# Optimization experiments

Hardware: AMD Instinct MI355X
Metric: run time of the kernel (lower is better)

Reference implementation:

```python
import jax, jax.numpy as jnp
import numpy as np

B, D, H, C, HALT_H, MAX_STEPS = 8192, 2048, 1024, 1000, 32, 10
EPS = 1e-08


def setup_inputs() -> dict:
    key = jax.random.key(0)
    ks = jax.random.split(key, 12)
    s = 0.02
    return {
        "x": jax.random.normal(ks[0], (B, D), jnp.float32),
        "enc_W": jax.random.normal(ks[1], (H, D), jnp.float32) * s,
        "enc_b": jnp.zeros((H,), jnp.float32),
        "ln_g": jnp.ones((H,), jnp.float32),
        "ln_b": jnp.zeros((H,), jnp.float32),
        "W_ih": jax.random.normal(ks[2], (3 * H, H), jnp.float32) * s,
        "W_hh": jax.random.normal(ks[3], (3 * H, H), jnp.float32) * s,
        "b_ih": jnp.zeros((3 * H,), jnp.float32),
        "b_hh": jnp.zeros((3 * H,), jnp.float32),
        "cls_W": jax.random.normal(ks[4], (C, H), jnp.float32) * s,
        "cls_b": jnp.zeros((C,), jnp.float32),
        "h1_W": jax.random.normal(ks[5], (HALT_H, H), jnp.float32) * s,
        "h1_b": jnp.zeros((HALT_H,), jnp.float32),
        "h2_W": jax.random.normal(ks[6], (1, HALT_H), jnp.float32) * s,
        "h2_b": jnp.zeros((1,), jnp.float32),
    }


def _forward(x, enc_W, enc_b, ln_g, ln_b, W_ih, W_hh, b_ih, b_hh,
             cls_W, cls_b, h1_W, h1_b, h2_W, h2_b):
    # encoder: Linear -> LayerNorm -> GELU (exact)
    z = x @ enc_W.T + enc_b
    mu = jnp.mean(z, axis=-1, keepdims=True)
    var = jnp.var(z, axis=-1, keepdims=True)
    z = (z - mu) * jax.lax.rsqrt(var + 1e-05) * ln_g + ln_b
    h0 = jax.nn.gelu(z, approximate=False)

    def step(h, _):
        gi = h @ W_ih.T + b_ih   # GRUCell with input = hidden
        gh = h @ W_hh.T + b_hh
        gi_r, gi_z, gi_n = jnp.split(gi, 3, axis=-1)
        gh_r, gh_z, gh_n = jnp.split(gh, 3, axis=-1)
        r = jax.nn.sigmoid(gi_r + gh_r)
        zt = jax.nn.sigmoid(gi_z + gh_z)
        n = jnp.tanh(gi_n + r * gh_n)
        h_new = (1.0 - zt) * n + zt * h
        logits = h_new @ cls_W.T + cls_b                         # [B, C]
        halt = jax.nn.sigmoid(
            jax.nn.relu(h_new @ h1_W.T + h1_b) @ h2_W.T + h2_b
        )[:, 0]                                                   # [B]
        return h_new, (logits, halt)

    _, (logits_steps, halt_steps) = jax.lax.scan(step, h0, None, length=MAX_STEPS)
    logits_stack = jnp.transpose(logits_steps, (1, 0, 2))  # [B, T, C]
    halts_stack = jnp.transpose(halt_steps, (1, 0))        # [B, T]

    log_not_halt = jnp.log(1.0 - halts_stack + EPS)
    cumsum_log = jnp.cumsum(log_not_halt, axis=1)
    cumsum_shifted = jnp.concatenate(
        [jnp.zeros((halts_stack.shape[0], 1), halts_stack.dtype), cumsum_log[:, :-1]], axis=1)
    halt_dist = halts_stack * jnp.exp(cumsum_shifted)
    remainder = 1.0 - jnp.sum(halt_dist, axis=1, keepdims=True)
    halt_dist = jnp.concatenate(
        [halt_dist[:, :-1], halt_dist[:, -1:] + jnp.maximum(remainder, 0.0)], axis=1)

    weighted_logits = jnp.sum(halt_dist[:, :, None] * logits_stack, axis=1)  # [B, C]
    step_indices = jnp.arange(1, MAX_STEPS + 1, dtype=weighted_logits.dtype)
    expected_steps = jnp.sum(halt_dist * step_indices, axis=1)
    probs = jax.nn.softmax(weighted_logits, axis=1)
    softmax_conf = jnp.max(probs, axis=1)
    comp_uncertainty = expected_steps / MAX_STEPS
    confidence = 0.7 * softmax_conf + 0.3 * (1.0 - comp_uncertainty)
    return (weighted_logits, probs, confidence, softmax_conf,
            expected_steps, halt_dist, comp_uncertainty)


def reference(x, enc_W, enc_b, ln_g, ln_b, W_ih, W_hh, b_ih, b_hh,
              cls_W, cls_b, h1_W, h1_b, h2_W, h2_b):
    return _forward(x, enc_W, enc_b, ln_g, ln_b, W_ih, W_hh, b_ih, b_hh,
                    cls_W, cls_b, h1_W, h1_b, h2_W, h2_b)
```

## Files before the change

### kernel.cpp

```cpp
#include <hip/hip_runtime.h>
#include <hip/hip_bf16.h>

#define B_ 8192
#define D_ 2048
#define H_ 1024
#define C_ 1000
#define NSTEP 10

typedef __attribute__((ext_vector_type(8))) short short8;
typedef __attribute__((ext_vector_type(4))) float f32x4;

__device__ __forceinline__ f32x4 mfma16x16(short8 a, short8 b, f32x4 c) {
  return __builtin_amdgcn_mfma_f32_16x16x32_bf16(a, b, c, 0, 0, 0);
}

__device__ __forceinline__ void async16(void* lds_uniform, const void* gsrc) {
  __builtin_amdgcn_global_load_lds(
      (const __attribute__((address_space(1))) void*)gsrc,
      (__attribute__((address_space(3))) void*)lds_uniform, 16, 0, 0);
}

__device__ __forceinline__ float sigm(float x) { return 1.0f / (1.0f + __expf(-x)); }
__device__ __forceinline__ float tanh_fast(float x) { return 1.0f - 2.0f / (__expf(2.0f * x) + 1.0f); }
__device__ __forceinline__ float b2f(short s) {
  union { unsigned u; float f; } v; v.u = ((unsigned)(unsigned short)s) << 16; return v.f;
}
__device__ __forceinline__ unsigned short f2us(float f) {
  __hip_bfloat16 h = __float2bfloat16(f); return *(unsigned short*)&h;
}

__device__ __forceinline__ int swz(int row, int slot) {
  return (row << 7) + (((slot) ^ (row & 7)) << 4);
}

__global__ void cvt_bf16_pad(const float* __restrict__ src, __hip_bfloat16* __restrict__ dst,
                             int n4, int nsrc4) {
  int i = blockIdx.x * 256 + threadIdx.x;
  if (i >= n4) return;
  float4 v = make_float4(0.f, 0.f, 0.f, 0.f);
  if (i < nsrc4) v = ((const float4*)src)[i];
  ((ushort4*)dst)[i] = make_ushort4(f2us(v.x), f2us(v.y), f2us(v.z), f2us(v.w));
}

__global__ void cvt_gates(const float* __restrict__ Wih, const float* __restrict__ Whh,
                          __hip_bfloat16* __restrict__ dst) {
  const int i = blockIdx.x * 256 + threadIdx.x;
  const int per_gate = (H_ * H_) / 4;
  const int gate = i / per_gate, rem = i - gate * per_gate;
  float4 v;
  if (gate == 0) {
    float4 a = ((const float4*)Wih)[rem], b = ((const float4*)Whh)[rem];
    v = make_float4(a.x + b.x, a.y + b.y, a.z + b.z, a.w + b.w);
  } else if (gate == 1) {
    float4 a = ((const float4*)Wih)[per_gate + rem], b = ((const float4*)Whh)[per_gate + rem];
    v = make_float4(a.x + b.x, a.y + b.y, a.z + b.z, a.w + b.w);
  } else if (gate == 2) {
    v = ((const float4*)Wih)[2 * per_gate + rem];
  } else {
    v = ((const float4*)Whh)[2 * per_gate + rem];
  }
  ((ushort4*)dst)[i] = make_ushort4(f2us(v.x), f2us(v.y), f2us(v.z), f2us(v.w));
}

template<int EPI>
__global__ __launch_bounds__(256, 2)
void gemm_bt(const __hip_bfloat16* __restrict__ A, int lda,
             const __hip_bfloat16* __restrict__ Bt, int ldb, int K,
             const float* __restrict__ bias,
             float* __restrict__ out, int out_ld, int ncol,
             const float* __restrict__ wrow) {
  __shared__ __hip_bfloat16 sA[128 * 64];
  __shared__ __hip_bfloat16 sB[128 * 64];
  const int tid = threadIdx.x;
  const int wave = tid >> 6, lane = tid & 63;
  const int m0 = blockIdx.x * 128, n0 = blockIdx.y * 128;
  const int wm = (wave >> 1) * 64, wn = (wave & 1) * 64;
  const int lr = lane & 15;
  const int g4 = lane >> 4;
  const int srow = wave * 8 + (lane >> 3);
  const int scol = ((lane & 7) ^ ((lane >> 3) & 7)) * 8;

  f32x4 acc[4][4] = {};

  const __hip_bfloat16* Asrc = A + (size_t)(m0 + srow) * lda + scol;
  const __hip_bfloat16* Bsrc = Bt + (size_t)(n0 + srow) * ldb + scol;

  for (int k0 = 0; k0 < K; k0 += 64) {
#pragma unroll
    for (int c = 0; c < 4; ++c) {
      async16((char*)sA + c * 4096 + wave * 1024, Asrc + (size_t)(c * 32) * lda + k0);
      async16((char*)sB + c * 4096 + wave * 1024, Bsrc + (size_t)(c * 32) * ldb + k0);
    }
    __syncthreads();
#pragma unroll
    for (int ks = 0; ks < 2; ++ks) {
      const int slot = ks * 4 + g4;
      short8 af[4], bfr[4];
#pragma unroll
      for (int i = 0; i < 4; ++i) {
        af[i]  = *(const short8*)((const char*)sA + swz(wm + i * 16 + lr, slot));
        bfr[i] = *(const short8*)((const char*)sB + swz(wn + i * 16 + lr, slot));
      }
#pragma unroll
      for (int i = 0; i < 4; ++i)
#pragma unroll
        for (int j = 0; j < 4; ++j)
          acc[i][j] = mfma16x16(af[i], bfr[j], acc[i][j]);
    }
    __syncthreads();
  }

  const int rbase = (lane >> 4) * 4;
  const int cbase = lane & 15;
#pragma unroll
  for (int i = 0; i < 4; ++i) {
#pragma unroll
    for (int r = 0; r < 4; ++r) {
      const int grow = m0 + wm + i * 16 + rbase + r;
      if (EPI == 1) {
        const float ws = wrow[grow];
#pragma unroll
        for (int j = 0; j < 4; ++j) {
          const int gcol = n0 + wn + j * 16 + cbase;
          if (gcol < ncol)
            out[(size_t)grow * out_ld + gcol] = acc[i][j][r] + bias[gcol] * ws;
        }
      } else {
#pragma unroll
        for (int j = 0; j < 4; ++j) {
          const int gcol = n0 + wn + j * 16 + cbase;
          out[(size_t)grow * out_ld + gcol] = acc[i][j][r] + bias[gcol];
        }
      }
    }
  }
}

__global__ __launch_bounds__(512, 4)
void gemm_gru(const __hip_bfloat16* __restrict__ A,
              const __hip_bfloat16* __restrict__ Wc4,
              const float* __restrict__ b_ih, const float* __restrict__ b_hh,
              __hip_bfloat16* __restrict__ hnewb) {
  __shared__ __hip_bfloat16 sA[256 * 64];
  __shared__ __hip_bfloat16 sB[4 * 32 * 64];
  const int tid = threadIdx.x, wave = tid >> 6, lane = tid & 63;
  const int m0 = blockIdx.x * 256, n0 = blockIdx.y * 32;
  const int wm = (wave >> 1) * 64;
  const int wc = wave & 1;
  const int lr = lane & 15;
  const int g4 = lane >> 4;
  const int scol = ((lane & 7) ^ ((lane >> 3) & 7)) * 8;

  f32x4 acc[4][4] = {};

  const __hip_bfloat16* Asrc = A + (size_t)(m0 + wave * 8 + (lane >> 3)) * H_ + scol;
  const __hip_bfloat16* Bsrc = Wc4 + ((size_t)(wave >> 2) << 20)
                             + (size_t)(n0 + (wave & 3) * 8 + (lane >> 3)) * H_ + scol;

  for (int k0 = 0; k0 < H_; k0 += 64) {
#pragma unroll
    for (int c = 0; c < 4; ++c)
      async16((char*)sA + c * 8192 + wave * 1024, Asrc + (size_t)(c * 64) * H_ + k0);
#pragma unroll
    for (int i = 0; i < 2; ++i)
      async16((char*)sB + i * 8192 + wave * 1024, Bsrc + ((size_t)(i * 2) << 20) + k0);
    __syncthreads();
#pragma unroll
    for (int ks = 0; ks < 2; ++ks) {
      const int slot = ks * 4 + g4;
      short8 af[4];
#pragma unroll
      for (int mi = 0; mi < 4; ++mi)
        af[mi] = *(const short8*)((const char*)sA + swz(wm + mi * 16 + lr, slot));
      short8 bf[4];
#pragma unroll
      for (int g = 0; g < 4; ++g)
        bf[g] = *(const short8*)((const char*)sB + g * 4096 + swz(wc * 16 + lr, slot));
#pragma unroll
      for (int mi = 0; mi < 4; ++mi)
#pragma unroll
        for (int g = 0; g < 4; ++g)
          acc[mi][g] = mfma16x16(af[mi], bf[g], acc[mi][g]);
    }
    __syncthreads();
  }

  const int rbase = (lane >> 4) * 4;
  const int cbase = lane & 15;
  const int gcol = n0 + wc * 16 + cbase;
  const float brz = b_ih[gcol] + b_hh[gcol];
  const float bzz = b_ih[H_ + gcol] + b_hh[H_ + gcol];
  const float bin = b_ih[2 * H_ + gcol];
  const float bhn = b_hh[2 * H_ + gcol];
#pragma unroll
  for (int mi = 0; mi < 4; ++mi) {
#pragma unroll
    for (int r = 0; r < 4; ++r) {
      const int grow = m0 + wm + mi * 16 + rbase + r;
      const size_t idx = (size_t)grow * H_ + gcol;
      const float rg = sigm(acc[mi][0][r] + brz);
      const float zg = sigm(acc[mi][1][r] + bzz);
      const float ng = tanh_fast(acc[mi][2][r] + bin + rg * (acc[mi][3][r] + bhn));
      const float hv = b2f(*(const short*)(A + idx));
      hnewb[idx] = __float2bfloat16((1.0f - zg) * ng + zg * hv);
    }
  }
}

__global__ void ln_gelu(const float* __restrict__ z, const float* __restrict__ g,
                        const float* __restrict__ bta, __hip_bfloat16* __restrict__ hb) {
  const int row = blockIdx.x, t = threadIdx.x;
  __shared__ float rs[4], rs2[4];
  float4 v = ((const float4*)(z + (size_t)row * H_))[t];
  float s = v.x + v.y + v.z + v.w;
  float s2 = v.x * v.x + v.y * v.y + v.z * v.z + v.w * v.w;
#pragma unroll
  for (int off = 32; off; off >>= 1) {
    s += __shfl_down(s, off);
    s2 += __shfl_down(s2, off);
  }
  if ((t & 63) == 0) { rs[t >> 6] = s; rs2[t >> 6] = s2; }
  __syncthreads();
  const float mu = (rs[0] + rs[1] + rs[2] + rs[3]) * (1.0f / H_);
  const float var = (rs2[0] + rs2[1] + rs2[2] + rs2[3]) * (1.0f / H_) - mu * mu;
  const float rstd = rsqrtf(var + 1e-5f);
  float4 gg = ((const float4*)g)[t];
  float4 bb = ((const float4*)bta)[t];
  float o[4], res[4];
  o[0] = (v.x - mu) * rstd * gg.x + bb.x;
  o[1] = (v.y - mu) * rstd * gg.y + bb.y;
  o[2] = (v.z - mu) * rstd * gg.z + bb.z;
  o[3] = (v.w - mu) * rstd * gg.w + bb.w;
#pragma unroll
  for (int k = 0; k < 4; ++k)
    res[k] = 0.5f * o[k] * (1.0f + erff(o[k] * 0.70710678118654752f));
  ((ushort4*)(hb + (size_t)row * H_))[t] =
      make_ushort4(f2us(res[0]), f2us(res[1]), f2us(res[2]), f2us(res[3]));
}

__global__ __launch_bounds__(256, 4)
void halt_mlp2(const __hip_bfloat16* __restrict__ hb,
               const __hip_bfloat16* __restrict__ h1Wb,
               const float* __restrict__ h1b, const float* __restrict__ h2W,
               const float* __restrict__ h2b,
               float* __restrict__ cum, float* __restrict__ psum,
               float* __restrict__ esum, float* __restrict__ wsum,
               float* __restrict__ out_hd, float* __restrict__ out_es,
               float* __restrict__ out_cu, int step) {
  __shared__ float part[2][2][64][8];
  const int tid = threadIdx.x, wave = tid >> 6, lane = tid & 63;
  const int rowgrp = wave >> 1, khalf = wave & 1;
  const int m0 = (blockIdx.x * 2 + rowgrp) * 16;
  const int lr = lane & 15, lk = (lane >> 4) * 8;

  const __hip_bfloat16* Arow = hb + (size_t)(m0 + lr) * H_ + khalf * 512 + lk;
  const __hip_bfloat16* B0 = h1Wb + (size_t)lr * H_ + khalf * 512 + lk;
  const __hip_bfloat16* B1 = h1Wb + (size_t)(16 + lr) * H_ + khalf * 512 + lk;
  f32x4 acc0 = {}, acc1 = {};
#pragma unroll 4
  for (int kk = 0; kk < 512; kk += 32) {
    short8 a  = *(const short8*)(Arow + kk);
    short8 b0 = *(const short8*)(B0 + kk);
    short8 b1 = *(const short8*)(B1 + kk);
    acc0 = mfma16x16(a, b0, acc0);
    acc1 = mfma16x16(a, b1, acc1);
  }
#pragma unroll
  for (int q = 0; q < 4; ++q) {
    part[rowgrp][khalf][lane][q]     = acc0[q];
    part[rowgrp][khalf][lane][4 + q] = acc1[q];
  }
  __syncthreads();
  if (khalf) return;

  const float w2a = h2W[lr], w2b = h2W[16 + lr];
  const float b1a = h1b[lr], b1b = h1b[16 + lr];
  float p[4];
#pragma unroll
  for (int q = 0; q < 4; ++q) {
    const float u0 = part[rowgrp][0][lane][q]     + part[rowgrp][1][lane][q]     + b1a;
    const float u1 = part[rowgrp][0][lane][4 + q] + part[rowgrp][1][lane][4 + q] + b1b;
    p[q] = fmaxf(u0, 0.f) * w2a + fmaxf(u1, 0.f) * w2b;
  }
#pragma unroll
  for (int m = 1; m < 16; m <<= 1) {
#pragma unroll
    for (int q = 0; q < 4; ++q) p[q] += __shfl_xor(p[q], m);
  }
  if (lr == 0) {
    const float b2 = h2b[0];
#pragma unroll
    for (int q = 0; q < 4; ++q) {
      const int rl = (lane >> 4) * 4 + q;
      const int row = m0 + rl;
      const float halt = 1.f / (1.f + expf(-(p[q] + b2)));
      float c  = (step == 0) ? 0.f : cum[row];
      float ps = (step == 0) ? 0.f : psum[row];
      float es = (step == 0) ? 0.f : esum[row];
      const float pt = halt * expf(c);
      float w;
      if (step == NSTEP - 1) {
        w = pt + fmaxf(1.f - (ps + pt), 0.f);
        es += w * (float)NSTEP;
        out_es[row] = es;
        out_cu[row] = es * (1.0f / NSTEP);
        wsum[row] = ps + w;
      } else {
        w = pt;
        es += w * (float)(step + 1);
        cum[row] = c + logf(1.f - halt + 1e-8f);
        psum[row] = ps + pt;
        esum[row] = es;
      }
      out_hd[(size_t)row * NSTEP + step] = w;
    }
  }
}

__global__ void hw_final(const __hip_bfloat16* __restrict__ hstack,
                         const float* __restrict__ out_hd,
                         __hip_bfloat16* __restrict__ hwb) {
  const int t = threadIdx.x;
  const int row = blockIdx.x * 4 + (t >> 6);
  const int c0 = (t & 63) * 16;
  const float* hd = out_hd + (size_t)row * NSTEP;
  float accv[16] = {};
#pragma unroll
  for (int s = 0; s < NSTEP; ++s) {
    const float w = hd[s];
    const short8* p = (const short8*)(hstack + ((size_t)(s + 1) * B_ + row) * H_ + c0);
    short8 a0 = p[0], a1 = p[1];
#pragma unroll
    for (int q = 0; q < 8; ++q) accv[q] += w * b2f(a0[q]);
#pragma unroll
    for (int q = 0; q < 8; ++q) accv[8 + q] += w * b2f(a1[q]);
  }
  short8 r0, r1;
#pragma unroll
  for (int q = 0; q < 8; ++q) { r0[q] = (short)f2us(accv[q]); r1[q] = (short)f2us(accv[8 + q]); }
  short8* dst = (short8*)(hwb + (size_t)row * H_ + c0);
  dst[0] = r0; dst[1] = r1;
}

__global__ void finalize(const float* __restrict__ wl, const float* __restrict__ es,
                         float* __restrict__ probs, float* __restrict__ conf,
                         float* __restrict__ sconf) {
  const int row = blockIdx.x, t = threadIdx.x;
  __shared__ float red[4], red2[4];
  float4 v = make_float4(-1e30f, -1e30f, -1e30f, -1e30f);
  float m = -1e30f;
  if (t < 250) {
    v = ((const float4*)(wl + (size_t)row * C_))[t];
    m = fmaxf(fmaxf(v.x, v.y), fmaxf(v.z, v.w));
  }
#pragma unroll
  for (int off = 32; off; off >>= 1) m = fmaxf(m, __shfl_down(m, off));
  if ((t & 63) == 0) red[t >> 6] = m;
  __syncthreads();
  m = fmaxf(fmaxf(red[0], red[1]), fmaxf(red[2], red[3]));
  float4 e = make_float4(0.f, 0.f, 0.f, 0.f);
  float s = 0.f;
  if (t < 250) {
    e.x = expf(v.x - m); e.y = expf(v.y - m); e.z = expf(v.z - m); e.w = expf(v.w - m);
    s = e.x + e.y + e.z + e.w;
  }
#pragma unroll
  for (int off = 32; off; off >>= 1) s += __shfl_down(s, off);
  if ((t & 63) == 0) red2[t >> 6] = s;
  __syncthreads();
  s = red2[0] + red2[1] + red2[2] + red2[3];
  const float inv = 1.0f / s;
  if (t < 250)
    ((float4*)(probs + (size_t)row * C_))[t] = make_float4(e.x * inv, e.y * inv, e.z * inv, e.w * inv);
  if (t == 0) {
    sconf[row] = inv;
    conf[row] = 0.7f * inv + 0.3f * (1.0f - es[row] * (1.0f / NSTEP));
  }
}

extern "C" void kernel_launch(void* const* d_in, const int* in_sizes, int n_in,
                              void* d_out, int out_size, void* d_ws, size_t ws_size,
                              hipStream_t stream) {
  (void)in_sizes; (void)n_in; (void)out_size; (void)ws_size;
  const float* x     = (const float*)d_in[0];
  const float* enc_W = (const float*)d_in[1];
  const float* enc_b = (const float*)d_in[2];
  const float* ln_g  = (const float*)d_in[3];
  const float* ln_b  = (const float*)d_in[4];
  const float* W_ih  = (const float*)d_in[5];
  const float* W_hh  = (const float*)d_in[6];
  const float* b_ih  = (const float*)d_in[7];
  const float* b_hh  = (const float*)d_in[8];
  const float* cls_W = (const float*)d_in[9];
  const float* cls_b = (const float*)d_in[10];
  const float* h1_W  = (const float*)d_in[11];
  const float* h1_b  = (const float*)d_in[12];
  const float* h2_W  = (const float*)d_in[13];
  const float* h2_b  = (const float*)d_in[14];

  char* wsp = (char*)d_ws;
  auto carve = [&](size_t n) { char* p = wsp; wsp += (n + 255) & ~(size_t)255; return p; };
  __hip_bfloat16* Wc4b   = (__hip_bfloat16*)carve((size_t)4 * H_ * H_ * 2);
  __hip_bfloat16* clsWb  = (__hip_bfloat16*)carve((size_t)1024 * 1024 * 2);
  __hip_bfloat16* encWb  = (__hip_bfloat16*)carve((size_t)H_ * D_ * 2);
  __hip_bfloat16* h1Wb   = (__hip_bfloat16*)carve((size_t)32 * H_ * 2);
  __hip_bfloat16* hstack = (__hip_bfloat16*)carve((size_t)(NSTEP + 1) * B_ * H_ * 2);
  float* cum  = (float*)carve((size_t)B_ * 4);
  float* psum = (float*)carve((size_t)B_ * 4);
  float* esum = (float*)carve((size_t)B_ * 4);
  float* wsum = (float*)carve((size_t)B_ * 4);

  const size_t SLOT = (size_t)B_ * H_;
  float* z            = (float*)(hstack + SLOT);
  __hip_bfloat16* xb  = hstack + 3 * SLOT;
  __hip_bfloat16* hwb = hstack;

  float* out = (float*)d_out;
  float* out_wl    = out;
  float* out_probs = out + (size_t)B_ * C_;
  float* out_conf  = out + (size_t)2 * B_ * C_;
  float* out_sconf = out_conf + B_;
  float* out_es    = out_sconf + B_;
  float* out_hd    = out_es + B_;
  float* out_cu    = out_hd + (size_t)B_ * NSTEP;

  dim3 blk(256);
  { int n4 = B_ * D_ / 4;       cvt_bf16_pad<<<(n4 + 255) / 256, blk, 0, stream>>>(x, xb, n4, n4); }
  { int n4 = H_ * D_ / 4;       cvt_bf16_pad<<<(n4 + 255) / 256, blk, 0, stream>>>(enc_W, encWb, n4, n4); }
  { int n4 = 4 * H_ * H_ / 4;   cvt_gates<<<(n4 + 255) / 256, blk, 0, stream>>>(W_ih, W_hh, Wc4b); }
  { int n4 = 1024 * 1024 / 4;   cvt_bf16_pad<<<(n4 + 255) / 256, blk, 0, stream>>>(cls_W, clsWb, n4, C_ * H_ / 4); }
  { int n4 = 32 * H_ / 4;       cvt_bf16_pad<<<(n4 + 255) / 256, blk, 0, stream>>>(h1_W, h1Wb, n4, n4); }

  gemm_bt<0><<<dim3(B_ / 128, H_ / 128), blk, 0, stream>>>(
      xb, D_, encWb, D_, D_, enc_b, z, H_, H_, nullptr);
  ln_gelu<<<B_, blk, 0, stream>>>(z, ln_g, ln_b, hstack);

  for (int step = 0; step < NSTEP; ++step) {
    const __hip_bfloat16* hprev = hstack + (size_t)step * SLOT;
    __hip_bfloat16* hnext = hstack + (size_t)(step + 1) * SLOT;
    gemm_gru<<<dim3(B_ / 256, H_ / 32), dim3(512), 0, stream>>>(
        hprev, Wc4b, b_ih, b_hh, hnext);
    halt_mlp2<<<B_ / 32, blk, 0, stream>>>(
        hnext, h1Wb, h1_b, h2_W, h2_b, cum, psum, esum, wsum,
        out_hd, out_es, out_cu, step);
  }

  hw_final<<<B_ / 4, blk, 0, stream>>>(hstack, out_hd, hwb);

  gemm_bt<1><<<dim3(B_ / 128, 1024 / 128), blk, 0, stream>>>(
      hwb, H_, clsWb, H_, H_, cls_b, out_wl, C_, C_, wsum);

  finalize<<<B_, blk, 0, stream>>>(out_wl, out_es, out_probs, out_conf, out_sconf);
}
```

Before: 974.0 us.

## Pipeline GRU gate GEMM with 4-stage async LDS ring and split MFMA phases

Replaces the single-buffered K loop (64-wide tiles, two syncthreads per tile) in the GRU gate GEMM with a 4-deep ring of 32-wide K tiles. Async global-to-LDS loads are issued three tiles ahead and throttled with explicit vmcnt waits and raw s_barrier. MFMA work is split into two halves interleaved with LDS reads and staging, with s_setprio raised around the MFMAs. The goal is to hide global load latency behind compute. In exchange, LDS use grows to 96KB and launch bounds drop to one block per CU, so occupancy falls and correctness now depends on the hand-tuned waitcnt counts.

```diff
diff --git a/kernel.cpp b/kernel.cpp
--- a/kernel.cpp
+++ b/kernel.cpp
@@ -136,53 +136,82 @@
   }
 }
 
-__global__ __launch_bounds__(512, 4)
+__global__ __launch_bounds__(512, 1)
 void gemm_gru(const __hip_bfloat16* __restrict__ A,
               const __hip_bfloat16* __restrict__ Wc4,
               const float* __restrict__ b_ih, const float* __restrict__ b_hh,
               __hip_bfloat16* __restrict__ hnewb) {
-  __shared__ __hip_bfloat16 sA[256 * 64];
-  __shared__ __hip_bfloat16 sB[4 * 32 * 64];
+  __shared__ __align__(16) char lds[4 * 24576];
   const int tid = threadIdx.x, wave = tid >> 6, lane = tid & 63;
   const int m0 = blockIdx.x * 256, n0 = blockIdx.y * 32;
   const int wm = (wave >> 1) * 64;
   const int wc = wave & 1;
-  const int lr = lane & 15;
-  const int g4 = lane >> 4;
-  const int scol = ((lane & 7) ^ ((lane >> 3) & 7)) * 8;
+  const int lr = lane & 15, g4 = lane >> 4;
+  const int soff = ((g4 ^ ((lr >> 1) & 3)) << 4);
 
   f32x4 acc[4][4] = {};
 
-  const __hip_bfloat16* Asrc = A + (size_t)(m0 + wave * 8 + (lane >> 3)) * H_ + scol;
-  const __hip_bfloat16* Bsrc = Wc4 + ((size_t)(wave >> 2) << 20)
-                             + (size_t)(n0 + (wave & 3) * 8 + (lane >> 3)) * H_ + scol;
-
-  for (int k0 = 0; k0 < H_; k0 += 64) {
-#pragma unroll
-    for (int c = 0; c < 4; ++c)
-      async16((char*)sA + c * 8192 + wave * 1024, Asrc + (size_t)(c * 64) * H_ + k0);
-#pragma unroll
-    for (int i = 0; i < 2; ++i)
-      async16((char*)sB + i * 8192 + wave * 1024, Bsrc + ((size_t)(i * 2) << 20) + k0);
-    __syncthreads();
-#pragma unroll
-    for (int ks = 0; ks < 2; ++ks) {
-      const int slot = ks * 4 + g4;
-      short8 af[4];
-#pragma unroll
-      for (int mi = 0; mi < 4; ++mi)
-        af[mi] = *(const short8*)((const char*)sA + swz(wm + mi * 16 + lr, slot));
-      short8 bf[4];
-#pragma unroll
-      for (int g = 0; g < 4; ++g)
-        bf[g] = *(const short8*)((const char*)sB + g * 4096 + swz(wc * 16 + lr, slot));
-#pragma unroll
-      for (int mi = 0; mi < 4; ++mi)
-#pragma unroll
-        for (int g = 0; g < 4; ++g)
-          acc[mi][g] = mfma16x16(af[mi], bf[g], acc[mi][g]);
-    }
-    __syncthreads();
+  const int scol = (((lane & 3) ^ ((lane >> 3) & 3)) << 3);
+  const __hip_bfloat16* AsrcS = A + (size_t)(m0 + wave * 16 + (lane >> 2)) * H_ + scol;
+  const __hip_bfloat16* BsrcS = Wc4 + ((size_t)(wave >> 1) << 20)
+      + (size_t)(n0 + (wave & 1) * 16 + (lane >> 2)) * H_ + scol;
+
+  auto stageA = [&](char* buf, int kt) {
+#pragma unroll
+    for (int c = 0; c < 2; ++c)
+      async16(buf + c * 8192 + wave * 1024, AsrcS + (size_t)(c * 128) * H_ + kt * 32);
+  };
+  auto stageB = [&](char* buf, int kt) {
+    async16(buf + 16384 + wave * 1024, BsrcS + kt * 32);
+  };
+
+  stageA(lds, 0);              stageB(lds, 0);
+  stageA(lds + 24576, 1);      stageB(lds + 24576, 1);
+  stageA(lds + 2 * 24576, 2);  stageB(lds + 2 * 24576, 2);
+  asm volatile("s_waitcnt vmcnt(6)" ::: "memory");
+  __builtin_amdgcn_s_barrier();
+
+#pragma unroll 4
+  for (int t = 0; t < 32; ++t) {
+    char* rb = lds + (t & 3) * 24576;
+    char* sb = lds + ((t + 3) & 3) * 24576;
+    const bool dostage = (t + 3 < 32);
+
+    short8 af[4], bf01[2];
+#pragma unroll
+    for (int mi = 0; mi < 4; ++mi)
+      af[mi] = *(const short8*)(rb + (wm + mi * 16 + lr) * 64 + soff);
+#pragma unroll
+    for (int g = 0; g < 2; ++g)
+      bf01[g] = *(const short8*)(rb + 16384 + g * 2048 + (wc * 16 + lr) * 64 + soff);
+    if (dostage) stageA(sb, t + 3);
+    __builtin_amdgcn_s_barrier();
+    __builtin_amdgcn_s_setprio(1);
+#pragma unroll
+    for (int mi = 0; mi < 4; ++mi) {
+      acc[mi][0] = mfma16x16(af[mi], bf01[0], acc[mi][0]);
+      acc[mi][1] = mfma16x16(af[mi], bf01[1], acc[mi][1]);
+    }
+    __builtin_amdgcn_s_setprio(0);
+    __builtin_amdgcn_s_barrier();
+
+    short8 bf23[2];
+#pragma unroll
+    for (int g = 0; g < 2; ++g)
+      bf23[g] = *(const short8*)(rb + 16384 + (2 + g) * 2048 + (wc * 16 + lr) * 64 + soff);
+    if (dostage) stageB(sb, t + 3);
+    __builtin_amdgcn_s_barrier();
+    __builtin_amdgcn_s_setprio(1);
+#pragma unroll
+    for (int mi = 0; mi < 4; ++mi) {
+      acc[mi][2] = mfma16x16(af[mi], bf23[0], acc[mi][2]);
+      acc[mi][3] = mfma16x16(af[mi], bf23[1], acc[mi][3]);
+    }
+    __builtin_amdgcn_s_setprio(0);
+    if (t < 29)       asm volatile("s_waitcnt vmcnt(6)" ::: "memory");
+    else if (t == 29) asm volatile("s_waitcnt vmcnt(3)" ::: "memory");
+    else if (t == 30) asm volatile("s_waitcnt vmcnt(0)" ::: "memory");
+    __builtin_amdgcn_s_barrier();
   }
 
   const int rbase = (lane >> 4) * 4;
```

Result: slower. 1.082 ms (+11.1%).

## Load GRU A operands directly from global and batch halt MLP across steps

Applied to the files above, without the earlier changes.

The GRU GEMM now uses 128x32 tiles with 256 threads, stages only the weight tile in LDS, and reads the hidden-state A fragments straight from global memory. The grid is reordered so blocks sharing the same rows are adjacent, which should keep those rows in cache. The per-step halt MLP launches are replaced by one batched launch over all steps plus a small per-row kernel that runs the ponder recurrence, cutting 9 launches and serialized small kernels. The risk is that unstaged global A loads add latency and traffic that LDS staging used to hide.

```diff
diff --git a/kernel.cpp b/kernel.cpp
--- a/kernel.cpp
+++ b/kernel.cpp
@@ -136,42 +136,38 @@
   }
 }
 
-__global__ __launch_bounds__(512, 4)
+__global__ __launch_bounds__(256, 4)
 void gemm_gru(const __hip_bfloat16* __restrict__ A,
               const __hip_bfloat16* __restrict__ Wc4,
               const float* __restrict__ b_ih, const float* __restrict__ b_hh,
               __hip_bfloat16* __restrict__ hnewb) {
-  __shared__ __hip_bfloat16 sA[256 * 64];
   __shared__ __hip_bfloat16 sB[4 * 32 * 64];
   const int tid = threadIdx.x, wave = tid >> 6, lane = tid & 63;
-  const int m0 = blockIdx.x * 256, n0 = blockIdx.y * 32;
-  const int wm = (wave >> 1) * 64;
-  const int wc = wave & 1;
+  const int n0 = blockIdx.x * 32, m0 = blockIdx.y * 128;
+  const int wr = wave >> 1, wc = wave & 1;
   const int lr = lane & 15;
   const int g4 = lane >> 4;
+  const int lk = g4 * 8;
+  const int srow = lane >> 3;
   const int scol = ((lane & 7) ^ ((lane >> 3) & 7)) * 8;
 
   f32x4 acc[4][4] = {};
 
-  const __hip_bfloat16* Asrc = A + (size_t)(m0 + wave * 8 + (lane >> 3)) * H_ + scol;
-  const __hip_bfloat16* Bsrc = Wc4 + ((size_t)(wave >> 2) << 20)
-                             + (size_t)(n0 + (wave & 3) * 8 + (lane >> 3)) * H_ + scol;
+  const __hip_bfloat16* Bsrc = Wc4 + (size_t)(n0 + wave * 8 + srow) * H_ + scol;
+  const __hip_bfloat16* Arow = A + (size_t)(m0 + wr * 64 + lr) * H_;
 
   for (int k0 = 0; k0 < H_; k0 += 64) {
 #pragma unroll
-    for (int c = 0; c < 4; ++c)
-      async16((char*)sA + c * 8192 + wave * 1024, Asrc + (size_t)(c * 64) * H_ + k0);
-#pragma unroll
-    for (int i = 0; i < 2; ++i)
-      async16((char*)sB + i * 8192 + wave * 1024, Bsrc + ((size_t)(i * 2) << 20) + k0);
+    for (int g = 0; g < 4; ++g)
+      async16((char*)sB + g * 4096 + wave * 1024, Bsrc + ((size_t)g << 20) + k0);
     __syncthreads();
 #pragma unroll
     for (int ks = 0; ks < 2; ++ks) {
+      short8 af[4];
+#pragma unroll
+      for (int mi = 0; mi < 4; ++mi)
+        af[mi] = *(const short8*)(Arow + (size_t)(mi * 16) * H_ + k0 + ks * 32 + lk);
       const int slot = ks * 4 + g4;
-      short8 af[4];
-#pragma unroll
-      for (int mi = 0; mi < 4; ++mi)
-        af[mi] = *(const short8*)((const char*)sA + swz(wm + mi * 16 + lr, slot));
       short8 bf[4];
 #pragma unroll
       for (int g = 0; g < 4; ++g)
@@ -196,7 +192,7 @@
   for (int mi = 0; mi < 4; ++mi) {
 #pragma unroll
     for (int r = 0; r < 4; ++r) {
-      const int grow = m0 + wm + mi * 16 + rbase + r;
+      const int grow = m0 + wr * 64 + mi * 16 + rbase + r;
       const size_t idx = (size_t)grow * H_ + gcol;
       const float rg = sigm(acc[mi][0][r] + brz);
       const float zg = sigm(acc[mi][1][r] + bzz);
@@ -239,16 +235,15 @@
 }
 
 __global__ __launch_bounds__(256, 4)
-void halt_mlp2(const __hip_bfloat16* __restrict__ hb,
-               const __hip_bfloat16* __restrict__ h1Wb,
-               const float* __restrict__ h1b, const float* __restrict__ h2W,
-               const float* __restrict__ h2b,
-               float* __restrict__ cum, float* __restrict__ psum,
-               float* __restrict__ esum, float* __restrict__ wsum,
-               float* __restrict__ out_hd, float* __restrict__ out_es,
-               float* __restrict__ out_cu, int step) {
+void halt_mlp_all(const __hip_bfloat16* __restrict__ hstack,
+                  const __hip_bfloat16* __restrict__ h1Wb,
+                  const float* __restrict__ h1b, const float* __restrict__ h2W,
+                  const float* __restrict__ h2b,
+                  float* __restrict__ hbuf) {
   __shared__ float part[2][2][64][8];
   const int tid = threadIdx.x, wave = tid >> 6, lane = tid & 63;
+  const int tstep = blockIdx.y;
+  const __hip_bfloat16* hb = hstack + (size_t)(tstep + 1) * B_ * H_;
   const int rowgrp = wave >> 1, khalf = wave & 1;
   const int m0 = (blockIdx.x * 2 + rowgrp) * 16;
   const int lr = lane & 15, lk = (lane >> 4) * 8;
@@ -291,30 +286,39 @@
     const float b2 = h2b[0];
 #pragma unroll
     for (int q = 0; q < 4; ++q) {
-      const int rl = (lane >> 4) * 4 + q;
-      const int row = m0 + rl;
-      const float halt = 1.f / (1.f + expf(-(p[q] + b2)));
-      float c  = (step == 0) ? 0.f : cum[row];
-      float ps = (step == 0) ? 0.f : psum[row];
-      float es = (step == 0) ? 0.f : esum[row];
-      const float pt = halt * expf(c);
-      float w;
-      if (step == NSTEP - 1) {
-        w = pt + fmaxf(1.f - (ps + pt), 0.f);
-        es += w * (float)NSTEP;
-        out_es[row] = es;
-        out_cu[row] = es * (1.0f / NSTEP);
-        wsum[row] = ps + w;
-      } else {
-        w = pt;
-        es += w * (float)(step + 1);
-        cum[row] = c + logf(1.f - halt + 1e-8f);
-        psum[row] = ps + pt;
-        esum[row] = es;
-      }
-      out_hd[(size_t)row * NSTEP + step] = w;
-    }
-  }
+      const int row = m0 + (lane >> 4) * 4 + q;
+      hbuf[(size_t)row * NSTEP + tstep] = 1.f / (1.f + expf(-(p[q] + b2)));
+    }
+  }
+}
+
+__global__ void ponder_rec(const float* __restrict__ hbuf,
+                           float* __restrict__ out_hd, float* __restrict__ out_es,
+                           float* __restrict__ out_cu, float* __restrict__ wsum) {
+  const int row = blockIdx.x * 256 + threadIdx.x;
+  const float* hp = hbuf + (size_t)row * NSTEP;
+  float c = 0.f, ps = 0.f, es = 0.f;
+  float hd[NSTEP];
+#pragma unroll
+  for (int t = 0; t < NSTEP; ++t) {
+    const float halt = hp[t];
+    const float pt = halt * expf(c);
+    float w;
+    if (t == NSTEP - 1) {
+      w = pt + fmaxf(1.f - (ps + pt), 0.f);
+    } else {
+      w = pt;
+      c += logf(1.f - halt + 1e-8f);
+      ps += pt;
+    }
+    es += w * (float)(t + 1);
+    hd[t] = w;
+  }
+#pragma unroll
+  for (int t = 0; t < NSTEP; ++t) out_hd[(size_t)row * NSTEP + t] = hd[t];
+  out_es[row] = es;
+  out_cu[row] = es * (1.0f / NSTEP);
+  wsum[row] = ps + hd[NSTEP - 1];
 }
 
 __global__ void hw_final(const __hip_bfloat16* __restrict__ hstack,
@@ -409,6 +413,8 @@
   float* psum = (float*)carve((size_t)B_ * 4);
   float* esum = (float*)carve((size_t)B_ * 4);
   float* wsum = (float*)carve((size_t)B_ * 4);
+  float* hbuf = (float*)carve((size_t)B_ * NSTEP * 4);
+  (void)cum; (void)psum; (void)esum;
 
   const size_t SLOT = (size_t)B_ * H_;
   float* z            = (float*)(hstack + SLOT);
@@ -438,12 +444,13 @@
   for (int step = 0; step < NSTEP; ++step) {
     const __hip_bfloat16* hprev = hstack + (size_t)step * SLOT;
     __hip_bfloat16* hnext = hstack + (size_t)(step + 1) * SLOT;
-    gemm_gru<<<dim3(B_ / 256, H_ / 32), dim3(512), 0, stream>>>(
+    gemm_gru<<<dim3(H_ / 32, B_ / 128), blk, 0, stream>>>(
         hprev, Wc4b, b_ih, b_hh, hnext);
-    halt_mlp2<<<B_ / 32, blk, 0, stream>>>(
-        hnext, h1Wb, h1_b, h2_W, h2_b, cum, psum, esum, wsum,
-        out_hd, out_es, out_cu, step);
-  }
+  }
+
+  halt_mlp_all<<<dim3(B_ / 32, NSTEP), blk, 0, stream>>>(
+      hstack, h1Wb, h1_b, h2_W, h2_b, hbuf);
+  ponder_rec<<<B_ / 256, blk, 0, stream>>>(hbuf, out_hd, out_es, out_cu, wsum);
 
   hw_final<<<B_ / 4, blk, 0, stream>>>(hstack, out_hd, hwb);
 
```

New measurement: 1.600 ms. 1.64x slower.
